# Kernel optimization log

Measured on AMD Instinct MI355X. Metric: run time of the kernel, lower is better.

Reference implementation:

```python
import jax, jax.numpy as jnp
import numpy as np

DIM, HEADS, HID, L = 256, 8, 1024, 17
DI, DS, DTR = 2 * DIM, 4, DIM // 16  # mamba: d_inner, d_state, dt_rank
B = 4096
HOP = np.array([0, 1, 4, 7, 2, 5, 8, 3, 6, 9, 11, 14, 10, 12, 15, 13, 16])
GRAPH = np.array([0, 1, 4, 7, 2, 5, 8, 3, 6, 9, 12, 10, 13, 15, 11, 14, 16])
# Human3.6M 17-joint skeleton, symmetric-normalized adjacency with self loops
_EDGES = [(0,1),(1,2),(2,3),(0,4),(4,5),(5,6),(0,7),(7,8),(8,9),(9,10),(8,11),(11,12),(12,13),(8,14),(14,15),(15,16)]
_A = np.eye(L, dtype=np.float32)
for i, j in _EDGES:
    _A[i, j] = _A[j, i] = 1.0
_d = _A.sum(1)
A_HAT = jnp.asarray(_A / np.sqrt(np.outer(_d, _d)))


def ln(x, g, b):
    m = x.mean(-1, keepdims=True)
    v = ((x - m) ** 2).mean(-1, keepdims=True)
    return (x - m) * jax.lax.rsqrt(v + 1e-5) * g + b


def mamba(u, in_proj_w, conv_w, conv_b, x_proj_w, dt_proj_w, dt_proj_b, A_log, Dp, out_proj_w):
    # u: [B,L,DIM]
    xz = u @ in_proj_w                      # [B,L,2*DI]
    xm, z = jnp.split(xz, 2, axis=-1)
    xm = jax.nn.silu(xm * conv_w + conv_b)  # depthwise conv, kernel=1
    dbl = xm @ x_proj_w                     # [B,L,DTR+2*DS]
    dt = jax.nn.softplus(dbl[..., :DTR] @ dt_proj_w + dt_proj_b)  # [B,L,DI]
    Bm = dbl[..., DTR:DTR + DS]             # [B,L,DS]
    Cm = dbl[..., DTR + DS:]                # [B,L,DS]
    A = -jnp.exp(A_log)                     # [DI,DS]
    dA = jnp.exp(dt[..., None] * A)                               # [B,L,DI,DS]
    dBx = dt[..., None] * Bm[:, :, None, :] * xm[..., None]       # [B,L,DI,DS]

    def step(h, inp):
        dA_t, dBx_t, C_t = inp
        h = dA_t * h + dBx_t
        y = jnp.einsum('bds,bs->bd', h, C_t)
        return h, y

    h0 = jnp.zeros((u.shape[0], DI, DS), u.dtype)
    _, ys = jax.lax.scan(step, h0, (dA.transpose(1, 0, 2, 3), dBx.transpose(1, 0, 2, 3), Cm.transpose(1, 0, 2)))
    y = ys.transpose(1, 0, 2) + Dp * xm
    y = y * jax.nn.silu(z)
    return y @ out_proj_w


def setup_inputs() -> dict:
    key = jax.random.key(0)
    ks = iter(jax.random.split(key, 32))
    r = lambda shape, s=0.02: jax.random.normal(next(ks), shape, jnp.float32) * s
    inp = {
        'x': jax.random.normal(next(ks), (B, L, DIM), jnp.float32),
        # GCN sub-block
        'gcn_ln_g': jnp.ones((DIM,)), 'gcn_ln_b': jnp.zeros((DIM,)),
        'gcn_w1': r((DIM, 2 * DIM)), 'gcn_b1': jnp.zeros((2 * DIM,)),
        'gcn_w2': r((2 * DIM, DIM)), 'gcn_b2': jnp.zeros((DIM,)),
        # SSM sub-block
        'bp_embed': r((1, 5, DIM)),
        'ssm_ln_g': jnp.ones((DIM,)), 'ssm_ln_b': jnp.zeros((DIM,)),
        'in_proj_w': r((DIM, 2 * DI)),
        'conv_w': jnp.ones((DI,)), 'conv_b': jnp.zeros((DI,)),
        'x_proj_w': r((DI, DTR + 2 * DS)),
        'dt_proj_w': r((DTR, DI)), 'dt_proj_b': jnp.zeros((DI,)),
        'A_log': jnp.log(jnp.broadcast_to(jnp.arange(1, DS + 1, dtype=jnp.float32), (DI, DS))),
        'Dp': jnp.ones((DI,)),
        'out_proj_w': r((DI, DIM)),
        # Transformer sub-block
        'ln1_g': jnp.ones((DIM,)), 'ln1_b': jnp.zeros((DIM,)),
        'qkv_w': r((DIM, 3 * DIM)),
        'attn_proj_w': r((DIM, DIM)), 'attn_proj_b': jnp.zeros((DIM,)),
        'ln2_g': jnp.ones((DIM,)), 'ln2_b': jnp.zeros((DIM,)),
        'mlp_w1': r((DIM, HID)), 'mlp_b1': jnp.zeros((HID,)),
        'mlp_w2': r((HID, DIM)), 'mlp_b2': jnp.zeros((DIM,)),
    }
    return inp


def reference(x, gcn_ln_g, gcn_ln_b, gcn_w1, gcn_b1, gcn_w2, gcn_b2,
              bp_embed, ssm_ln_g, ssm_ln_b, in_proj_w, conv_w, conv_b,
              x_proj_w, dt_proj_w, dt_proj_b, A_log, Dp, out_proj_w,
              ln1_g, ln1_b, qkv_w, attn_proj_w, attn_proj_b,
              ln2_g, ln2_b, mlp_w1, mlp_b1, mlp_w2, mlp_b2):
    # ---- GCN sub-block (2-layer graph conv over 17-joint skeleton) ----
    res = x
    h = ln(x, gcn_ln_g, gcn_ln_b)
    h = jnp.einsum('ij,bjd->bid', A_HAT, h) @ gcn_w1 + gcn_b1
    h = jax.nn.gelu(h)
    h = jnp.einsum('ij,bjd->bid', A_HAT, h) @ gcn_w2 + gcn_b2
    x = res + h  # Block residual
    # ---- PoseSSM sub-block ----
    res = x
    bp = bp_embed[0]  # [5,DIM]
    x_bpe = jnp.concatenate([bp[:3], bp[:3], bp[:3], bp[:1], bp[3:], bp[:1], bp[3:], bp[3:]], axis=0)  # [17,DIM]
    xs = x[:, HOP, :] + x_bpe
    xs = ln(xs, ssm_ln_g, ssm_ln_b)
    xs = mamba(xs, in_proj_w, conv_w, conv_b, x_proj_w, dt_proj_w, dt_proj_b, A_log, Dp, out_proj_w)
    xs = xs[:, GRAPH, :]
    x = res + xs   # residual inside PoseSSM_module
    x = x + res    # residual in Block
    # ---- Transformer sub-block ----
    res = x
    t = ln(x, ln1_g, ln1_b)
    qkv = (t @ qkv_w).reshape(t.shape[0], L, 3, HEADS, DIM // HEADS)
    q, k, v = qkv[:, :, 0], qkv[:, :, 1], qkv[:, :, 2]  # [B,L,H,dh]
    scale = (DIM // HEADS) ** -0.5
    att = jax.nn.softmax(jnp.einsum('bqhd,bkhd->bhqk', q, k) * scale, axis=-1)
    o = jnp.einsum('bhqk,bkhd->bqhd', att, v).reshape(t.shape[0], L, DIM)
    o = o @ attn_proj_w + attn_proj_b
    x1 = x + o
    m = ln(x1, ln2_g, ln2_b)
    m = jax.nn.gelu(m @ mlp_w1 + mlp_b1) @ mlp_w2 + mlp_b2
    x2 = x1 + m
    return x2 + res
```

## Files before the change

kernel.cpp:

```cpp
#include <hip/hip_runtime.h>
#include <hip/hip_bf16.h>
#include <math.h>


#define LSEQ 17
#define RS 256
#define TS 264
#define SS 520
#define SCS 40
#define NTHR 1024
#define NWAVE 16

typedef unsigned short u16;
typedef __attribute__((ext_vector_type(8))) short short8;
typedef __attribute__((ext_vector_type(4))) float f32x4;

__device__ __forceinline__ float b2f(u16 u) {
    union { unsigned int i; float f; } x; x.i = ((unsigned int)u) << 16; return x.f;
}
__device__ __forceinline__ u16 f2b(float f) {
    union { float f; unsigned int i; } x; x.f = f;
    unsigned int r = x.i + 0x7FFFu + ((x.i >> 16) & 1u);
    return (u16)(r >> 16);
}
__device__ __forceinline__ float gelu_t(float x) {
    float u = 1.5957691216057308f * (x + 0.044715f * x * x * x);
    return x / (1.0f + __expf(-u));
}
__device__ __forceinline__ float siluf(float x) { return x / (1.0f + __expf(-x)); }
__device__ __forceinline__ float softplusf(float x) {
    return (x > 20.0f) ? x : __logf(1.0f + __expf(x));
}

__device__ const int HOPA[17]   = {0,1,4,7,2,5,8,3,6,9,11,14,10,12,15,13,16};
__device__ const int GRAPHA[17] = {0,1,4,7,2,5,8,3,6,9,12,10,13,15,11,14,16};
__device__ const int BPEI[17]   = {0,1,2,0,1,2,0,1,2,0,3,4,0,3,4,3,4};

#define OFF_GCN_W1   0
#define OFF_GCN_W2   131072
#define OFF_INPROJ   262144
#define OFF_OUTPROJ  524288
#define OFF_QKV      655360
#define OFF_ATTNPROJ 851968
#define OFF_MLP_W1   917504
#define OFF_MLP_W2   1179648
#define OFF_XPROJ    1441792

#define SM_R    0
#define SM_AC   34816
#define SM_T1   52768
#define SM_W5   70720
#define SM_U    106080
#define SMEM_BYTES 127840

struct Params {
    const float *x, *gcn_ln_g, *gcn_ln_b, *gcn_w1, *gcn_b1, *gcn_w2, *gcn_b2,
                *bp_embed, *ssm_ln_g, *ssm_ln_b, *in_proj_w, *conv_w, *conv_b,
                *x_proj_w, *dt_proj_w, *dt_proj_b, *A_log, *Dp, *out_proj_w,
                *ln1_g, *ln1_b, *qkv_w, *attn_proj_w, *attn_proj_b,
                *ln2_g, *ln2_b, *mlp_w1, *mlp_b1, *mlp_w2, *mlp_b2;
    const u16* wws;
    float* out;
};

__global__ __launch_bounds__(256) void prepack(Params P) {
    const int gid = blockIdx.x * 256 + threadIdx.x;
    const int cnt[9]  = {16384,16384,32768,16384,24576,8192,32768,32768,2048};
    const int Ns [9]  = {512,256,1024,256,768,256,1024,256,24};
    const int NPs[9]  = {512,256,1024,256,768,256,1024,256,32};
    const int offs[9] = {OFF_GCN_W1,OFF_GCN_W2,OFF_INPROJ,OFF_OUTPROJ,OFF_QKV,
                         OFF_ATTNPROJ,OFF_MLP_W1,OFF_MLP_W2,OFF_XPROJ};
    int e = 0, base = 0;
    while (e < 9 && gid >= base + cnt[e]) { base += cnt[e]; ++e; }
    if (e >= 9) return;
    const float* W;
    switch (e) {
        case 0: W = P.gcn_w1; break;      case 1: W = P.gcn_w2; break;
        case 2: W = P.in_proj_w; break;   case 3: W = P.out_proj_w; break;
        case 4: W = P.qkv_w; break;       case 5: W = P.attn_proj_w; break;
        case 6: W = P.mlp_w1; break;      case 7: W = P.mlp_w2; break;
        default: W = P.x_proj_w; break;
    }
    const int local = gid - base;
    const int lane = local & 63, frag = local >> 6;
    const int NT = NPs[e] >> 4;
    const int nt = frag % NT, kc = frag / NT;
    const int n = nt * 16 + (lane & 15);
    const int kbase = kc * 32 + (lane >> 4) * 8;
    u16 v[8];
    #pragma unroll
    for (int j = 0; j < 8; ++j)
        v[j] = (n < Ns[e]) ? f2b(W[(size_t)(kbase + j) * Ns[e] + n]) : (u16)0;
    u16* dst = (u16*)P.wws + offs[e] + ((size_t)frag * 64 + lane) * 8;
    *(short8*)dst = *(short8*)v;
}

template <int KT>
__device__ __forceinline__ void mfmaAcc3(f32x4 acc[3],
        const u16* __restrict__ act, int ldin,
        const u16* __restrict__ wbase, int NT, int nt0, int ntcnt, int kc0) {
    const int lane = threadIdx.x & 63, wv = threadIdx.x >> 6;
    const int m = lane & 15, quad = lane >> 4;
    const bool v2 = (m < 2);
    const int ntl = wv;
    if (ntl >= ntcnt) return;
    for (int kc = 0; kc < KT; ++kc) {
        const int ko = kc * 32 + quad * 8;
        short8 a0 = *(const short8*)(act + m * ldin + ko);
        short8 a1 = *(const short8*)(act + (16 + m) * ldin + ko);
        short8 a2 = {0,0,0,0,0,0,0,0};
        if (v2) a2 = *(const short8*)(act + (32 + m) * ldin + ko);
        const short8 b = *(const short8*)(wbase +
            ((size_t)((kc0 + kc) * NT + nt0 + ntl) * 64 + lane) * 8);
        acc[0] = __builtin_amdgcn_mfma_f32_16x16x32_bf16(a0, b, acc[0], 0, 0, 0);
        acc[1] = __builtin_amdgcn_mfma_f32_16x16x32_bf16(a1, b, acc[1], 0, 0, 0);
        acc[2] = __builtin_amdgcn_mfma_f32_16x16x32_bf16(a2, b, acc[2], 0, 0, 0);
    }
}

template <class Epi>
__device__ __forceinline__ void mfmaStore3(f32x4 acc[3], int ntcnt, Epi epi) {
    const int lane = threadIdx.x & 63, wv = threadIdx.x >> 6;
    const int col0 = lane & 15, quad = lane >> 4;
    const int ntl = wv;
    if (ntl >= ntcnt) return;
    const int cb = ntl * 16 + col0;
    #pragma unroll
    for (int r = 0; r < 4; ++r) epi(quad * 4 + r, cb, acc[0][r]);
    #pragma unroll
    for (int r = 0; r < 4; ++r) epi(16 + quad * 4 + r, cb, acc[1][r]);
    if (quad == 0) {
        epi(32, cb, acc[2][0]);
        epi(33, cb, acc[2][1]);
    }
}

template <int KT, class Epi>
__device__ __forceinline__ void gemm3(const u16* act, int ldin,
        const u16* wbase, int NT, int nt0, int ntcnt, Epi epi) {
    f32x4 acc[3];
    #pragma unroll
    for (int mt = 0; mt < 3; ++mt) acc[mt] = (f32x4){0.f,0.f,0.f,0.f};
    mfmaAcc3<KT>(acc, act, ldin, wbase, NT, nt0, ntcnt, 0);
    mfmaStore3(acc, ntcnt, epi);
}

__global__ __launch_bounds__(NTHR, 4) void fused_block(Params P) {
    extern __shared__ __align__(16) char smem[];
    float* R   = (float*)(smem + SM_R);
    u16*   AC  = (u16*)  (smem + SM_AC);
    u16*   T1  = (u16*)  (smem + SM_T1);
    u16*   W5  = (u16*)  (smem + SM_W5);
    float* Dbl = (float*)(smem + SM_U);
    u16*   SC  = (u16*)  (smem + SM_U);

    const int tid = threadIdx.x;
    const int lane = tid & 63, wv = tid >> 6;
    const float* __restrict__ xg = P.x + (size_t)blockIdx.x * (2 * LSEQ * 256);
    const u16* __restrict__ ws = P.wws;

    for (int i4 = tid; i4 < 34 * 64; i4 += NTHR) {
        int rr = i4 >> 6, d4 = (i4 & 63) * 4;
        f32x4 v = __builtin_nontemporal_load((const f32x4*)(xg + rr * 256 + d4));
        *(f32x4*)(R + rr * RS + d4) = v;
    }
    __syncthreads();

    auto ln34 = [&](auto ld, u16* dst, const float* g, const float* bb) {
        for (int rr = wv; rr < 34; rr += NWAVE) {
            float v[4], s = 0.f, s2 = 0.f;
            #pragma unroll
            for (int j = 0; j < 4; ++j) {
                v[j] = ld(rr, lane + 64 * j);
                s += v[j]; s2 += v[j] * v[j];
            }
            #pragma unroll
            for (int m = 1; m < 64; m <<= 1) {
                s  += __shfl_xor(s, m, 64);
                s2 += __shfl_xor(s2, m, 64);
            }
            float mean = s * (1.0f / 256.0f);
            float var  = s2 * (1.0f / 256.0f) - mean * mean;
            float rstd = rsqrtf(var + 1e-5f);
            #pragma unroll
            for (int j = 0; j < 4; ++j) {
                int d = lane + 64 * j;
                dst[rr * TS + d] = f2b((v[j] - mean) * rstd * g[d] + bb[d]);
            }
        }
    };
    auto gconvIP = [&](u16* buf, int stride, int width) {
        for (int u = tid; u < 2 * width; u += NTHR) {
            int e = u / width, d = u - e * width;
            u16* be = buf + e * LSEQ * stride;
            float c[17];
            #pragma unroll
            for (int j = 0; j < 17; ++j) c[j] = b2f(be[j * stride + d]);
            float o[17];
            o[0]  = 0.25f*c[0] + 0.28867513f*(c[1]+c[4]+c[7]);
            o[1]  = 0.28867513f*c[0] + 0.33333334f*(c[1]+c[2]);
            o[2]  = 0.33333334f*(c[1]+c[2]) + 0.40824829f*c[3];
            o[3]  = 0.40824829f*c[2] + 0.5f*c[3];
            o[4]  = 0.28867513f*c[0] + 0.33333334f*(c[4]+c[5]);
            o[5]  = 0.33333334f*(c[4]+c[5]) + 0.40824829f*c[6];
            o[6]  = 0.40824829f*c[5] + 0.5f*c[6];
            o[7]  = 0.28867513f*c[0] + 0.33333334f*c[7] + 0.25819889f*c[8];
            o[8]  = 0.25819889f*(c[7]+c[9]+c[11]+c[14]) + 0.2f*c[8];
            o[9]  = 0.25819889f*c[8] + 0.33333334f*c[9] + 0.40824829f*c[10];
            o[10] = 0.40824829f*c[9] + 0.5f*c[10];
            o[11] = 0.25819889f*c[8] + 0.33333334f*(c[11]+c[12]);
            o[12] = 0.33333334f*(c[11]+c[12]) + 0.40824829f*c[13];
            o[13] = 0.40824829f*c[12] + 0.5f*c[13];
            o[14] = 0.25819889f*c[8] + 0.33333334f*(c[14]+c[15]);
            o[15] = 0.33333334f*(c[14]+c[15]) + 0.40824829f*c[16];
            o[16] = 0.40824829f*c[15] + 0.5f*c[16];
            #pragma unroll
            for (int i = 0; i < 17; ++i) be[i * stride + d] = f2b(o[i]);
        }
    };

    ln34([&](int rr, int d) { return R[rr * RS + d]; }, AC, P.gcn_ln_g, P.gcn_ln_b);
    __syncthreads();
    gconvIP(AC, TS, 256);
    __syncthreads();
    gemm3<8>(AC, TS, ws + OFF_GCN_W1, 32, 0, 16,
        [&](int rr, int c, float v) { W5[rr * SS + c] = f2b(gelu_t(v + P.gcn_b1[c])); });
    gemm3<8>(AC, TS, ws + OFF_GCN_W1, 32, 16, 16,
        [&](int rr, int c, float v) { W5[rr * SS + 256 + c] = f2b(gelu_t(v + P.gcn_b1[256 + c])); });
    __syncthreads();
    gconvIP(W5, SS, 512);
    __syncthreads();
    gemm3<16>(W5, SS, ws + OFF_GCN_W2, 16, 0, 16,
        [&](int rr, int c, float v) { R[rr * RS + c] += v + P.gcn_b2[c]; });
    __syncthreads();

    for (int i = tid; i < 34 * 256; i += NTHR) {
        int rr = i >> 8, d = i & 255;
        int e = (rr >= 17), l = rr - e * 17;
        AC[rr * TS + d] = f2b(R[(e * 17 + HOPA[l]) * RS + d] + P.bp_embed[BPEI[l] * 256 + d]);
    }
    __syncthreads();
    ln34([&](int rr, int d) { return b2f(AC[rr * TS + d]); }, T1, P.ssm_ln_g, P.ssm_ln_b);
    __syncthreads();
    gemm3<8>(T1, TS, ws + OFF_INPROJ, 64, 0, 16,
        [&](int rr, int c, float v) { W5[rr * SS + c] = f2b(siluf(v * P.conv_w[c] + P.conv_b[c])); });
    gemm3<8>(T1, TS, ws + OFF_INPROJ, 64, 16, 16,
        [&](int rr, int c, float v) { W5[rr * SS + 256 + c] = f2b(siluf(v * P.conv_w[256 + c] + P.conv_b[256 + c])); });
    __syncthreads();
    gemm3<16>(W5, SS, ws + OFF_XPROJ, 2, 0, 2,
        [&](int rr, int c, float v) { if (c < 24) Dbl[rr * 24 + c] = v; });
    __syncthreads();
    {
        const int e = tid >> 9, d = tid & 511;
        const int rb = e * LSEQ;
        float wdt[16];
        #pragma unroll
        for (int r = 0; r < 16; ++r) wdt[r] = P.dt_proj_w[r * 512 + d];
        const float dtb = P.dt_proj_b[d];
        float Ar[4];
        #pragma unroll
        for (int s = 0; s < 4; ++s) Ar[s] = -__expf(P.A_log[d * 4 + s]);
        const float Dpd = P.Dp[d];
        float h0 = 0.f, h1 = 0.f, h2 = 0.f, h3 = 0.f;
        for (int t = 0; t < LSEQ; ++t) {
            const float* Dv = Dbl + (rb + t) * 24;
            float a = dtb;
            #pragma unroll
            for (int r = 0; r < 16; ++r) a += Dv[r] * wdt[r];
            float dt_ = softplusf(a);
            float xm = b2f(W5[(rb + t) * SS + d]);
            float p = dt_ * xm;
            h0 = __expf(dt_ * Ar[0]) * h0 + p * Dv[16];
            h1 = __expf(dt_ * Ar[1]) * h1 + p * Dv[17];
            h2 = __expf(dt_ * Ar[2]) * h2 + p * Dv[18];
            h3 = __expf(dt_ * Ar[3]) * h3 + p * Dv[19];
            float y = h0 * Dv[20] + h1 * Dv[21] + h2 * Dv[22] + h3 * Dv[23] + Dpd * xm;
            W5[(rb + t) * SS + d] = f2b(y);
        }
    }
    __syncthreads();
    gemm3<8>(T1, TS, ws + OFF_INPROJ, 64, 32, 16,
        [&](int rr, int c, float v) {
            float y = b2f(W5[rr * SS + c]);
            W5[rr * SS + c] = f2b(y * siluf(v));
        });
    gemm3<8>(T1, TS, ws + OFF_INPROJ, 64, 48, 16,
        [&](int rr, int c, float v) {
            float y = b2f(W5[rr * SS + 256 + c]);
            W5[rr * SS + 256 + c] = f2b(y * siluf(v));
        });
    __syncthreads();
    gemm3<16>(W5, SS, ws + OFF_OUTPROJ, 16, 0, 16,
        [&](int rr, int c, float v) { AC[rr * TS + c] = f2b(v); });
    __syncthreads();
    for (int i = tid; i < 34 * 256; i += NTHR) {
        int rr = i >> 8, d = i & 255;
        int e = (rr >= 17), l = rr - e * 17;
        R[rr * RS + d] = 2.0f * R[rr * RS + d] + b2f(AC[(e * 17 + GRAPHA[l]) * TS + d]);
    }
    __syncthreads();

    ln34([&](int rr, int d) { return R[rr * RS + d]; }, AC, P.ln1_g, P.ln1_b);
    __syncthreads();
    gemm3<8>(AC, TS, ws + OFF_QKV, 48, 0, 16,
        [&](int rr, int c, float v) { T1[rr * TS + c] = f2b(v); });
    gemm3<8>(AC, TS, ws + OFF_QKV, 48, 16, 16,
        [&](int rr, int c, float v) { W5[rr * SS + c] = f2b(v); });
    gemm3<8>(AC, TS, ws + OFF_QKV, 48, 32, 16,
        [&](int rr, int c, float v) { W5[rr * SS + 256 + c] = f2b(v); });
    __syncthreads();
    {
        const int e = wv >> 3, h = wv & 7, m16 = lane & 15, quad = lane >> 4;
        const int rb = e * LSEQ;
        const u16* qb = T1 + rb * TS + h * 32 + quad * 8;
        const u16* kb = W5 + rb * SS + h * 32 + quad * 8;
        short8 qa0 = *(const short8*)(qb + m16 * TS);
        short8 ka0 = *(const short8*)(kb + m16 * SS);
        short8 qa1 = {0,0,0,0,0,0,0,0}, ka1 = {0,0,0,0,0,0,0,0};
        if (m16 == 0) {
            qa1 = *(const short8*)(qb + 16 * TS);
            ka1 = *(const short8*)(kb + 16 * SS);
        }
        f32x4 s00 = {0.f,0.f,0.f,0.f}, s01 = s00, s10 = s00, s11 = s00;
        s00 = __builtin_amdgcn_mfma_f32_16x16x32_bf16(qa0, ka0, s00, 0, 0, 0);
        s01 = __builtin_amdgcn_mfma_f32_16x16x32_bf16(qa0, ka1, s01, 0, 0, 0);
        s10 = __builtin_amdgcn_mfma_f32_16x16x32_bf16(qa1, ka0, s10, 0, 0, 0);
        s11 = __builtin_amdgcn_mfma_f32_16x16x32_bf16(qa1, ka1, s11, 0, 0, 0);
        const float sc = 0.17677669529663687f;
        u16* sh = SC + wv * 17 * SCS;
        #pragma unroll
        for (int r = 0; r < 4; ++r) {
            int i = quad * 4 + r;
            sh[i * SCS + m16]      = f2b(s00[r] * sc);
            sh[i * SCS + 16 + m16] = f2b(s01[r] * sc);
        }
        if (quad == 0) {
            sh[16 * SCS + m16]      = f2b(s10[0] * sc);
            sh[16 * SCS + 16 + m16] = f2b(s11[0] * sc);
        }
    }
    __syncthreads();
    if (tid < 272) {
        u16* row = SC + tid * SCS;
        float e[17], mx = -3.0e38f, sum = 0.f;
        #pragma unroll
        for (int j = 0; j < 17; ++j) mx = fmaxf(mx, b2f(row[j]));
        #pragma unroll
        for (int j = 0; j < 17; ++j) { e[j] = __expf(b2f(row[j]) - mx); sum += e[j]; }
        float inv = 1.0f / sum;
        #pragma unroll
        for (int j = 0; j < 17; ++j) row[j] = f2b(e[j] * inv);
    }
    __syncthreads();
    {
        const int e = wv >> 3, h = wv & 7, m16 = lane & 15, quad = lane >> 4;
        const int rb = e * LSEQ;
        const u16* sh = SC + wv * 17 * SCS + quad * 8;
        short8 pa0 = *(const short8*)(sh + m16 * SCS);
        short8 pa1 = {0,0,0,0,0,0,0,0};
        if (m16 == 0) pa1 = *(const short8*)(sh + 16 * SCS);
        #pragma unroll
        for (int nt = 0; nt < 2; ++nt) {
            const u16* vbase = W5 + rb * SS + 256 + h * 32 + nt * 16 + m16;
            short8 vb;
            #pragma unroll
            for (int j = 0; j < 8; ++j) {
                int k = quad * 8 + j;
                vb[j] = (k < 17) ? (short)vbase[k * SS] : (short)0;
            }
            f32x4 o0 = {0.f,0.f,0.f,0.f}, o1 = o0;
            o0 = __builtin_amdgcn_mfma_f32_16x16x32_bf16(pa0, vb, o0, 0, 0, 0);
            o1 = __builtin_amdgcn_mfma_f32_16x16x32_bf16(pa1, vb, o1, 0, 0, 0);
            #pragma unroll
            for (int r = 0; r < 4; ++r) {
                int i = quad * 4 + r;
                AC[(rb + i) * TS + h * 32 + nt * 16 + m16] = f2b(o0[r]);
            }
            if (quad == 0)
                AC[(rb + 16) * TS + h * 32 + nt * 16 + m16] = f2b(o1[0]);
        }
    }
    __syncthreads();
    gemm3<8>(AC, TS, ws + OFF_ATTNPROJ, 16, 0, 16,
        [&](int rr, int c, float v) { T1[rr * TS + c] = f2b(v + P.attn_proj_b[c]); });
    __syncthreads();

    ln34([&](int rr, int d) { return R[rr * RS + d] + b2f(T1[rr * TS + d]); },
         AC, P.ln2_g, P.ln2_b);
    __syncthreads();
    {
        f32x4 accO[3];
        #pragma unroll
        for (int mt = 0; mt < 3; ++mt) accO[mt] = (f32x4){0.f,0.f,0.f,0.f};
        #pragma unroll
        for (int half = 0; half < 2; ++half) {
            #pragma unroll
            for (int sub = 0; sub < 2; ++sub) {
                const int base = half * 512 + sub * 256;
                gemm3<8>(AC, TS, ws + OFF_MLP_W1, 64, half * 32 + sub * 16, 16,
                    [&](int rr, int c, float v) {
                        W5[rr * SS + sub * 256 + c] = f2b(gelu_t(v + P.mlp_b1[base + c]));
                    });
            }
            __syncthreads();
            mfmaAcc3<16>(accO, W5, SS, ws + OFF_MLP_W2, 16, 0, 16, half * 16);
            __syncthreads();
        }
        float* outg = P.out + (size_t)blockIdx.x * (2 * LSEQ * 256);
        mfmaStore3(accO, 16, [&](int rr, int c, float v) {
            float r = v + P.mlp_b2[c] + 2.0f * R[rr * RS + c] + b2f(T1[rr * TS + c]);
            __builtin_nontemporal_store(r, outg + rr * 256 + c);
        });
    }
}

extern "C" void kernel_launch(void* const* d_in, const int* in_sizes, int n_in,
                              void* d_out, int out_size, void* d_ws, size_t ws_size,
                              hipStream_t stream) {
    (void)in_sizes; (void)n_in; (void)ws_size; (void)out_size;
    Params P;
    P.x           = (const float*)d_in[0];
    P.gcn_ln_g    = (const float*)d_in[1];
    P.gcn_ln_b    = (const float*)d_in[2];
    P.gcn_w1      = (const float*)d_in[3];
    P.gcn_b1      = (const float*)d_in[4];
    P.gcn_w2      = (const float*)d_in[5];
    P.gcn_b2      = (const float*)d_in[6];
    P.bp_embed    = (const float*)d_in[7];
    P.ssm_ln_g    = (const float*)d_in[8];
    P.ssm_ln_b    = (const float*)d_in[9];
    P.in_proj_w   = (const float*)d_in[10];
    P.conv_w      = (const float*)d_in[11];
    P.conv_b      = (const float*)d_in[12];
    P.x_proj_w    = (const float*)d_in[13];
    P.dt_proj_w   = (const float*)d_in[14];
    P.dt_proj_b   = (const float*)d_in[15];
    P.A_log       = (const float*)d_in[16];
    P.Dp          = (const float*)d_in[17];
    P.out_proj_w  = (const float*)d_in[18];
    P.ln1_g       = (const float*)d_in[19];
    P.ln1_b       = (const float*)d_in[20];
    P.qkv_w       = (const float*)d_in[21];
    P.attn_proj_w = (const float*)d_in[22];
    P.attn_proj_b = (const float*)d_in[23];
    P.ln2_g       = (const float*)d_in[24];
    P.ln2_b       = (const float*)d_in[25];
    P.mlp_w1      = (const float*)d_in[26];
    P.mlp_b1      = (const float*)d_in[27];
    P.mlp_w2      = (const float*)d_in[28];
    P.mlp_b2      = (const float*)d_in[29];
    P.wws         = (const u16*)d_ws;
    P.out         = (float*)d_out;
    static int smem_set = 0;
    if (!smem_set) {
        hipFuncSetAttribute(reinterpret_cast<const void*>(fused_block),
                            hipFuncAttributeMaxDynamicSharedMemorySize, SMEM_BYTES);
        smem_set = 1;
    }
    hipLaunchKernelGGL(prepack, dim3(712), dim3(256), 0, stream, P);
    hipLaunchKernelGGL(fused_block, dim3(2048), dim3(NTHR), SMEM_BYTES, stream, P);
}
```

Before: 790.0 us.

## Reorder GCN second graph conv after W2 and transpose V for vector loads

The second graph convolution is moved from the 512-wide hidden activation to after the W2 projection, using linearity (A·H·W = A·(H·W)), so it runs over 256 columns instead of 512 and is fused with the residual add and bias. Separately, V is written transposed into a new zero-padded shared buffer so the attention PV stage loads B fragments with one 16-byte read instead of eight strided scalar reads. The extra shared memory (about 28KB more) may lower occupancy. The W2 output is rounded to bf16 before the conv, which changes numerics slightly.

```diff
diff --git a/kernel.cpp b/kernel.cpp
--- a/kernel.cpp
+++ b/kernel.cpp
@@ -8,6 +8,7 @@
 #define TS 264
 #define SS 520
 #define SCS 40
+#define VTS 56
 #define NTHR 1024
 #define NWAVE 16
 
@@ -51,7 +52,8 @@
 #define SM_T1   52768
 #define SM_W5   70720
 #define SM_U    106080
-#define SMEM_BYTES 127840
+#define SM_VT   127840
+#define SMEM_BYTES 156512
 
 struct Params {
     const float *x, *gcn_ln_g, *gcn_ln_b, *gcn_w1, *gcn_b1, *gcn_w2, *gcn_b2,
@@ -153,6 +155,7 @@
     u16*   W5  = (u16*)  (smem + SM_W5);
     float* Dbl = (float*)(smem + SM_U);
     u16*   SC  = (u16*)  (smem + SM_U);
+    u16*   VT  = (u16*)  (smem + SM_VT);
 
     const int tid = threadIdx.x;
     const int lane = tid & 63, wv = tid >> 6;
@@ -189,13 +192,12 @@
             }
         }
     };
-    auto gconvIP = [&](u16* buf, int stride, int width) {
+    auto gconvCols = [&](int width, auto ldf, auto stf) {
         for (int u = tid; u < 2 * width; u += NTHR) {
             int e = u / width, d = u - e * width;
-            u16* be = buf + e * LSEQ * stride;
             float c[17];
             #pragma unroll
-            for (int j = 0; j < 17; ++j) c[j] = b2f(be[j * stride + d]);
+            for (int j = 0; j < 17; ++j) c[j] = ldf(e, j, d);
             float o[17];
             o[0]  = 0.25f*c[0] + 0.28867513f*(c[1]+c[4]+c[7]);
             o[1]  = 0.28867513f*c[0] + 0.33333334f*(c[1]+c[2]);
@@ -215,23 +217,27 @@
             o[15] = 0.33333334f*(c[14]+c[15]) + 0.40824829f*c[16];
             o[16] = 0.40824829f*c[15] + 0.5f*c[16];
             #pragma unroll
-            for (int i = 0; i < 17; ++i) be[i * stride + d] = f2b(o[i]);
+            for (int i = 0; i < 17; ++i) stf(e, i, d, o[i]);
         }
     };
 
     ln34([&](int rr, int d) { return R[rr * RS + d]; }, AC, P.gcn_ln_g, P.gcn_ln_b);
     __syncthreads();
-    gconvIP(AC, TS, 256);
+    gconvCols(256,
+        [&](int e, int j, int d) { return b2f(AC[(e * 17 + j) * TS + d]); },
+        [&](int e, int i, int d, float v) { AC[(e * 17 + i) * TS + d] = f2b(v); });
     __syncthreads();
     gemm3<8>(AC, TS, ws + OFF_GCN_W1, 32, 0, 16,
         [&](int rr, int c, float v) { W5[rr * SS + c] = f2b(gelu_t(v + P.gcn_b1[c])); });
     gemm3<8>(AC, TS, ws + OFF_GCN_W1, 32, 16, 16,
         [&](int rr, int c, float v) { W5[rr * SS + 256 + c] = f2b(gelu_t(v + P.gcn_b1[256 + c])); });
     __syncthreads();
-    gconvIP(W5, SS, 512);
-    __syncthreads();
     gemm3<16>(W5, SS, ws + OFF_GCN_W2, 16, 0, 16,
-        [&](int rr, int c, float v) { R[rr * RS + c] += v + P.gcn_b2[c]; });
+        [&](int rr, int c, float v) { AC[rr * TS + c] = f2b(v); });
+    __syncthreads();
+    gconvCols(256,
+        [&](int e, int j, int d) { return b2f(AC[(e * 17 + j) * TS + d]); },
+        [&](int e, int i, int d, float v) { R[(e * 17 + i) * RS + d] += v + P.gcn_b2[d]; });
     __syncthreads();
 
     for (int i = tid; i < 34 * 256; i += NTHR) {
@@ -301,13 +307,18 @@
     __syncthreads();
 
     ln34([&](int rr, int d) { return R[rr * RS + d]; }, AC, P.ln1_g, P.ln1_b);
+    for (int i = tid; i < (256 * VTS) / 2; i += NTHR)
+        ((unsigned int*)VT)[i] = 0u;
     __syncthreads();
     gemm3<8>(AC, TS, ws + OFF_QKV, 48, 0, 16,
         [&](int rr, int c, float v) { T1[rr * TS + c] = f2b(v); });
     gemm3<8>(AC, TS, ws + OFF_QKV, 48, 16, 16,
         [&](int rr, int c, float v) { W5[rr * SS + c] = f2b(v); });
     gemm3<8>(AC, TS, ws + OFF_QKV, 48, 32, 16,
-        [&](int rr, int c, float v) { W5[rr * SS + 256 + c] = f2b(v); });
+        [&](int rr, int c, float v) {
+            int e2 = (rr >= 17), t = rr - e2 * 17;
+            VT[c * VTS + e2 * 24 + t] = f2b(v);
+        });
     __syncthreads();
     {
         const int e = wv >> 3, h = wv & 7, m16 = lane & 15, quad = lane >> 4;
@@ -361,13 +372,9 @@
         if (m16 == 0) pa1 = *(const short8*)(sh + 16 * SCS);
         #pragma unroll
         for (int nt = 0; nt < 2; ++nt) {
-            const u16* vbase = W5 + rb * SS + 256 + h * 32 + nt * 16 + m16;
-            short8 vb;
-            #pragma unroll
-            for (int j = 0; j < 8; ++j) {
-                int k = quad * 8 + j;
-                vb[j] = (k < 17) ? (short)vbase[k * SS] : (short)0;
-            }
+            const int n = h * 32 + nt * 16 + m16;
+            short8 vb = {0,0,0,0,0,0,0,0};
+            if (quad < 3) vb = *(const short8*)(VT + n * VTS + e * 24 + quad * 8);
             f32x4 o0 = {0.f,0.f,0.f,0.f}, o1 = o0;
             o0 = __builtin_amdgcn_mfma_f32_16x16x32_bf16(pa0, vb, o0, 0, 0, 0);
             o1 = __builtin_amdgcn_mfma_f32_16x16x32_bf16(pa1, vb, o1, 0, 0, 0);
```

Measured after the change: 779.6 us. No clear change (-1.3%).
